# Kernel tuning notes

Measured on AMD Instinct MI355X. Metric: run time of the kernel, lower is better.

Reference implementation:

```python
import jax, jax.numpy as jnp
import numpy as np


def setup_inputs() -> dict:
    key = jax.random.key(0)
    k1, k2 = jax.random.split(key)
    B, N, M = 8, 8192, 8192
    source_points = jax.random.normal(k1, (B, N, 3), dtype=jnp.float32)
    target_points = jax.random.normal(k2, (B, M, 3), dtype=jnp.float32)
    return {"source_points": source_points, "target_points": target_points}


def reference(source_points, target_points):
    # dist: [B, N, M]  (same math as (x[:, :, None] - y[:, None]) ** 2 summed over coords)
    s_sq = jnp.sum(source_points ** 2, axis=-1)  # [B, N]
    t_sq = jnp.sum(target_points ** 2, axis=-1)  # [B, M]
    cross = jnp.einsum("bnd,bmd->bnm", source_points, target_points)  # [B, N, M]
    dist = s_sq[:, :, None] + t_sq[:, None, :] - 2.0 * cross
    min_s2t = jnp.min(dist, axis=2)  # [B, N] nearest target for each source point
    min_t2s = jnp.min(dist, axis=1)  # [B, M] nearest source for each target point
    chamfer = jnp.mean(min_s2t, axis=1) + jnp.mean(min_t2s, axis=1)  # [B]
    return chamfer
```

## Files before the change

kernel.cpp:

```cpp
#include <hip/hip_runtime.h>


typedef float f32x16 __attribute__((ext_vector_type(16)));
typedef short bf16x8 __attribute__((ext_vector_type(8)));

constexpr int BATCH  = 8;
constexpr int NPTS   = 8192;
constexpr int BLOCK  = 256;
constexpr int QTILE  = 256;
constexpr int NAF    = 2;
constexpr int QB     = NPTS / QTILE;
constexpr int DSPLIT = 4;
constexpr int DBR    = NPTS / DSPLIT;
constexpr int NT     = DBR / 32;
constexpr int NBLK   = QB * BATCH * 2 * DSPLIT;

constexpr size_t FRAG_N = (size_t)BATCH * NPTS * 2;
constexpr size_t SM_N   = (size_t)BATCH * NPTS;

static __device__ __forceinline__ unsigned umin2(unsigned a, unsigned b) {
    return a < b ? a : b;
}
static __device__ __forceinline__ unsigned umin3(unsigned a, unsigned b, unsigned c) {
    return umin2(a, umin2(b, c));
}
static __device__ __forceinline__ unsigned short bf16h(float f) {
    unsigned int u = __float_as_uint(f);
    u += 0x7fffu + ((u >> 16) & 1u);
    return (unsigned short)(u >> 16);
}
static __device__ __forceinline__ float bf16tof(unsigned short h) {
    return __uint_as_float(((unsigned int)h) << 16);
}
static __device__ __forceinline__ unsigned int pack2(unsigned short a, unsigned short b) {
    return (unsigned int)a | ((unsigned int)b << 16);
}

static __device__ __forceinline__ void make_bfrag(float px, float py, float pz,
                                                  uint4& p0, uint4& p1) {
    const unsigned short one = bf16h(1.0f);
    float nx = -px, ny = -py, nz = -pz;
    float ht = 0.5f * fmaf(px, px, fmaf(py, py, pz * pz));
    unsigned short nxh = bf16h(nx), nxl = bf16h(nx - bf16tof(nxh));
    unsigned short nyh = bf16h(ny), nyl = bf16h(ny - bf16tof(nyh));
    unsigned short nzh = bf16h(nz), nzl = bf16h(nz - bf16tof(nzh));
    unsigned short hh = bf16h(ht),  hl = bf16h(ht - bf16tof(hh));
    p0 = make_uint4(pack2(nxh, nxl), pack2(nxh, nyh),
                    pack2(nyl, nyh), pack2(nzh, nzl));
    p1 = make_uint4(pack2(nzh, one), pack2(one, hh),
                    pack2(hl, one), 0u);
}

__global__ __launch_bounds__(BLOCK) void chamfer_prep(
    const float* __restrict__ src, const float* __restrict__ tgt,
    uint4* __restrict__ fragS, uint4* __restrict__ fragT,
    unsigned int* __restrict__ mins, float* __restrict__ out)
{
    const int i = blockIdx.x * BLOCK + threadIdx.x;
    uint4 p0, p1;
    const float* tp = tgt + (size_t)i * 3;
    make_bfrag(tp[0], tp[1], tp[2], p0, p1);
    fragT[2 * i + 0] = p0;
    fragT[2 * i + 1] = p1;
    const float* sp = src + (size_t)i * 3;
    make_bfrag(sp[0], sp[1], sp[2], p0, p1);
    fragS[2 * i + 0] = p0;
    fragS[2 * i + 1] = p1;
    mins[i]        = 0x7f7f7f7fu;
    mins[SM_N + i] = 0x7f7f7f7fu;
    if (i < BATCH) out[i] = 0.0f;
}

__global__ __launch_bounds__(BLOCK, 2) void chamfer_nn(
    const float* __restrict__ src, const float* __restrict__ tgt,
    const uint4* __restrict__ fragS, const uint4* __restrict__ fragT,
    unsigned int* __restrict__ mins)
{
    const int tid  = threadIdx.x;
    const int lane = tid & 63;
    const int w    = tid >> 6;
    const int half = lane >> 5;
    const int l31  = lane & 31;

    const int lin  = blockIdx.x;
    const int rest = lin >> 3;
    const int qb   = rest & 31;
    const int p    = ((rest >> 5) << 3) | (lin & 7);
    const int b    = p & 7;
    const int z    = p >> 3;
    const int dir  = z >> 2;
    const int ds   = z & 3;

    const float* P  = dir ? tgt : src;
    const uint4* FB = dir ? fragS : fragT;

    const unsigned short one = bf16h(1.0f);
    bf16x8 af[NAF];
#pragma unroll
    for (int g = 0; g < NAF; g++) {
        const int q = qb * QTILE + w * (32 * NAF) + g * 32 + l31;
        const float* qp = P + ((size_t)b * NPTS + q) * 3;
        float qx = qp[0], qy = qp[1], qz = qp[2];
        float hq = 0.5f * fmaf(qx, qx, fmaf(qy, qy, qz * qz));
        unsigned short xh = bf16h(qx), xl = bf16h(qx - bf16tof(xh));
        unsigned short yh = bf16h(qy), yl = bf16h(qy - bf16tof(yh));
        unsigned short zh = bf16h(qz), zl = bf16h(qz - bf16tof(zh));
        unsigned short qh = bf16h(hq), ql = bf16h(hq - bf16tof(qh));
        bf16x8 a;
        if (half == 0) {
            a[0] = (short)xh; a[1] = (short)xh; a[2] = (short)xl;
            a[3] = (short)yh; a[4] = (short)yh; a[5] = (short)yl;
            a[6] = (short)zh; a[7] = (short)zh;
        } else {
            a[0] = (short)zl; a[1] = (short)qh; a[2] = (short)ql;
            a[3] = (short)one; a[4] = (short)one;
            a[5] = (short)one;
            a[6] = 0; a[7] = 0;
        }
        af[g] = a;
    }

    unsigned rmn0[16], rmn1[16];
#pragma unroll
    for (int r = 0; r < 16; r++) { rmn0[r] = 0x7f7f7f7fu; rmn1[r] = 0x7f7f7f7fu; }
    const f32x16 zz = {};

    const uint4* gp = FB + ((size_t)b * NPTS + (size_t)ds * DBR) * 2
                         + 2 * l31 + half;

    uint4 c0 = gp[0], c1 = gp[64];
    for (int t = 0; t < NT; t += 2) {
        bf16x8 b0 = __builtin_bit_cast(bf16x8, c0);
        bf16x8 b1 = __builtin_bit_cast(bf16x8, c1);
        if (t + 2 < NT) {
            c0 = gp[64 * (t + 2)];
            c1 = gp[64 * (t + 3)];
        }
        f32x16 a00 = __builtin_amdgcn_mfma_f32_32x32x16_bf16(af[0], b0, zz, 0, 0, 0);
        f32x16 a01 = __builtin_amdgcn_mfma_f32_32x32x16_bf16(af[0], b1, zz, 0, 0, 0);
        f32x16 a10 = __builtin_amdgcn_mfma_f32_32x32x16_bf16(af[1], b0, zz, 0, 0, 0);
        f32x16 a11 = __builtin_amdgcn_mfma_f32_32x32x16_bf16(af[1], b1, zz, 0, 0, 0);
#pragma unroll
        for (int r = 0; r < 16; r++) {
            rmn0[r] = umin3(rmn0[r], __float_as_uint(a00[r]), __float_as_uint(a01[r]));
            rmn1[r] = umin3(rmn1[r], __float_as_uint(a10[r]), __float_as_uint(a11[r]));
        }
    }

    unsigned int* M = mins + ((size_t)dir * BATCH + b) * NPTS;
    const int qbase = qb * QTILE + w * (32 * NAF);
#pragma unroll
    for (int r = 0; r < 16; r++) {
        unsigned a = rmn0[r], bv = rmn1[r];
#pragma unroll
        for (int off = 16; off > 0; off >>= 1) {
            a  = umin2(a,  (unsigned)__shfl_xor((int)a,  off, 64));
            bv = umin2(bv, (unsigned)__shfl_xor((int)bv, off, 64));
        }
        if (l31 == 0) {
            const int row = (r & 3) + 8 * (r >> 2) + 4 * half;
            atomicMin(&M[qbase + row],      a);
            atomicMin(&M[qbase + 32 + row], bv);
        }
    }
}

__global__ __launch_bounds__(BLOCK) void chamfer_final(
    const unsigned int* __restrict__ mins, float* __restrict__ out)
{
    const int seg = blockIdx.x;
    const int b   = blockIdx.y;
    const int tid = threadIdx.x;
    float acc = 0.0f;
#pragma unroll
    for (int k = 0; k < 8; k++) {
        const size_t i = (size_t)b * NPTS + seg * 2048 + k * BLOCK + tid;
        acc += fmaxf(__uint_as_float(mins[i]) - 1.0f, 0.0f)
             + fmaxf(__uint_as_float(mins[SM_N + i]) - 1.0f, 0.0f);
    }
    for (int off = 32; off > 0; off >>= 1) acc += __shfl_down(acc, off, 64);
    __shared__ float wsum[4];
    if ((tid & 63) == 0) wsum[tid >> 6] = acc;
    __syncthreads();
    if (tid == 0)
        atomicAdd(&out[b],
                  (wsum[0] + wsum[1] + wsum[2] + wsum[3]) * (2.0f / (float)NPTS));
}

extern "C" void kernel_launch(void* const* d_in, const int* in_sizes, int n_in,
                              void* d_out, int out_size, void* d_ws, size_t ws_size,
                              hipStream_t stream) {
    const float* src = (const float*)d_in[0];
    const float* tgt = (const float*)d_in[1];
    float* out = (float*)d_out;

    uint4* fragT        = (uint4*)d_ws;
    uint4* fragS        = fragT + FRAG_N;
    unsigned int* mins  = (unsigned int*)(fragS + FRAG_N);

    chamfer_prep<<<BATCH * NPTS / BLOCK, BLOCK, 0, stream>>>(
        src, tgt, fragS, fragT, mins, out);
    chamfer_nn<<<NBLK, BLOCK, 0, stream>>>(
        src, tgt, fragS, fragT, mins);
    chamfer_final<<<dim3(4, BATCH), BLOCK, 0, stream>>>(mins, out);
}
```

Before: 100.2 us.

## Compute both chamfer directions from a single distance pass with column minima

The kernel previously ran two separate passes over the distance matrix, one per direction. It now runs only source-to-target tiles, and also reduces each MFMA tile over its rows to get per-target-column minima. Those minima are merged into a shared-memory array through LDS atomics and then flushed to global memory with atomicMin. This halves the MFMA work and block count, at the cost of extra per-tile min trees, cross-half shuffles, LDS atomics and a shared buffer that may reduce occupancy.

```diff
diff --git a/kernel.cpp b/kernel.cpp
--- a/kernel.cpp
+++ b/kernel.cpp
@@ -13,7 +13,7 @@
 constexpr int DSPLIT = 4;
 constexpr int DBR    = NPTS / DSPLIT;
 constexpr int NT     = DBR / 32;
-constexpr int NBLK   = QB * BATCH * 2 * DSPLIT;
+constexpr int NBLK   = QB * BATCH * DSPLIT;
 
 constexpr size_t FRAG_N = (size_t)BATCH * NPTS * 2;
 constexpr size_t SM_N   = (size_t)BATCH * NPTS;
@@ -24,10 +24,20 @@
 static __device__ __forceinline__ unsigned umin3(unsigned a, unsigned b, unsigned c) {
     return umin2(a, umin2(b, c));
 }
+static __device__ __forceinline__ unsigned u(float f) { return __float_as_uint(f); }
+
+static __device__ __forceinline__ unsigned tree16u(const f32x16& a) {
+    unsigned m = umin3(u(a[0]), u(a[1]), u(a[2]));
+    m = umin3(m, u(a[3]),  u(a[4]));  m = umin3(m, u(a[5]),  u(a[6]));
+    m = umin3(m, u(a[7]),  u(a[8]));  m = umin3(m, u(a[9]),  u(a[10]));
+    m = umin3(m, u(a[11]), u(a[12])); m = umin3(m, u(a[13]), u(a[14]));
+    return umin2(m, u(a[15]));
+}
+
 static __device__ __forceinline__ unsigned short bf16h(float f) {
-    unsigned int u = __float_as_uint(f);
-    u += 0x7fffu + ((u >> 16) & 1u);
-    return (unsigned short)(u >> 16);
+    unsigned int v = __float_as_uint(f);
+    v += 0x7fffu + ((v >> 16) & 1u);
+    return (unsigned short)(v >> 16);
 }
 static __device__ __forceinline__ float bf16tof(unsigned short h) {
     return __uint_as_float(((unsigned int)h) << 16);
@@ -36,46 +46,35 @@
     return (unsigned int)a | ((unsigned int)b << 16);
 }
 
-static __device__ __forceinline__ void make_bfrag(float px, float py, float pz,
-                                                  uint4& p0, uint4& p1) {
+__global__ __launch_bounds__(BLOCK) void chamfer_prep(
+    const float* __restrict__ tgt, uint4* __restrict__ fragT,
+    unsigned int* __restrict__ mins, float* __restrict__ out)
+{
+    const int i = blockIdx.x * BLOCK + threadIdx.x;
     const unsigned short one = bf16h(1.0f);
+    const float* tp = tgt + (size_t)i * 3;
+    float px = tp[0], py = tp[1], pz = tp[2];
     float nx = -px, ny = -py, nz = -pz;
     float ht = 0.5f * fmaf(px, px, fmaf(py, py, pz * pz));
     unsigned short nxh = bf16h(nx), nxl = bf16h(nx - bf16tof(nxh));
     unsigned short nyh = bf16h(ny), nyl = bf16h(ny - bf16tof(nyh));
     unsigned short nzh = bf16h(nz), nzl = bf16h(nz - bf16tof(nzh));
     unsigned short hh = bf16h(ht),  hl = bf16h(ht - bf16tof(hh));
-    p0 = make_uint4(pack2(nxh, nxl), pack2(nxh, nyh),
-                    pack2(nyl, nyh), pack2(nzh, nzl));
-    p1 = make_uint4(pack2(nzh, one), pack2(one, hh),
-                    pack2(hl, one), 0u);
-}
-
-__global__ __launch_bounds__(BLOCK) void chamfer_prep(
-    const float* __restrict__ src, const float* __restrict__ tgt,
-    uint4* __restrict__ fragS, uint4* __restrict__ fragT,
-    unsigned int* __restrict__ mins, float* __restrict__ out)
-{
-    const int i = blockIdx.x * BLOCK + threadIdx.x;
-    uint4 p0, p1;
-    const float* tp = tgt + (size_t)i * 3;
-    make_bfrag(tp[0], tp[1], tp[2], p0, p1);
-    fragT[2 * i + 0] = p0;
-    fragT[2 * i + 1] = p1;
-    const float* sp = src + (size_t)i * 3;
-    make_bfrag(sp[0], sp[1], sp[2], p0, p1);
-    fragS[2 * i + 0] = p0;
-    fragS[2 * i + 1] = p1;
+    fragT[2 * i + 0] = make_uint4(pack2(nxh, nxl), pack2(nxh, nyh),
+                                  pack2(nyl, nyh), pack2(nzh, nzl));
+    fragT[2 * i + 1] = make_uint4(pack2(nzh, one), pack2(one, hh),
+                                  pack2(hl, one), 0u);
     mins[i]        = 0x7f7f7f7fu;
     mins[SM_N + i] = 0x7f7f7f7fu;
     if (i < BATCH) out[i] = 0.0f;
 }
 
 __global__ __launch_bounds__(BLOCK, 2) void chamfer_nn(
-    const float* __restrict__ src, const float* __restrict__ tgt,
-    const uint4* __restrict__ fragS, const uint4* __restrict__ fragT,
+    const float* __restrict__ src, const uint4* __restrict__ fragT,
     unsigned int* __restrict__ mins)
 {
+    __shared__ unsigned sht[DBR];
+
     const int tid  = threadIdx.x;
     const int lane = tid & 63;
     const int w    = tid >> 6;
@@ -87,19 +86,16 @@
     const int qb   = rest & 31;
     const int p    = ((rest >> 5) << 3) | (lin & 7);
     const int b    = p & 7;
-    const int z    = p >> 3;
-    const int dir  = z >> 2;
-    const int ds   = z & 3;
-
-    const float* P  = dir ? tgt : src;
-    const uint4* FB = dir ? fragS : fragT;
+    const int ds   = p >> 3;
+
+    for (int j = tid; j < DBR; j += BLOCK) sht[j] = 0x7f7f7f7fu;
 
     const unsigned short one = bf16h(1.0f);
     bf16x8 af[NAF];
 #pragma unroll
     for (int g = 0; g < NAF; g++) {
         const int q = qb * QTILE + w * (32 * NAF) + g * 32 + l31;
-        const float* qp = P + ((size_t)b * NPTS + q) * 3;
+        const float* qp = src + ((size_t)b * NPTS + q) * 3;
         float qx = qp[0], qy = qp[1], qz = qp[2];
         float hq = 0.5f * fmaf(qx, qx, fmaf(qy, qy, qz * qz));
         unsigned short xh = bf16h(qx), xl = bf16h(qx - bf16tof(xh));
@@ -125,8 +121,10 @@
     for (int r = 0; r < 16; r++) { rmn0[r] = 0x7f7f7f7fu; rmn1[r] = 0x7f7f7f7fu; }
     const f32x16 zz = {};
 
-    const uint4* gp = FB + ((size_t)b * NPTS + (size_t)ds * DBR) * 2
-                         + 2 * l31 + half;
+    const uint4* gp = fragT + ((size_t)b * NPTS + (size_t)ds * DBR) * 2
+                            + 2 * l31 + half;
+
+    __syncthreads();
 
     uint4 c0 = gp[0], c1 = gp[64];
     for (int t = 0; t < NT; t += 2) {
@@ -142,12 +140,20 @@
         f32x16 a11 = __builtin_amdgcn_mfma_f32_32x32x16_bf16(af[1], b1, zz, 0, 0, 0);
 #pragma unroll
         for (int r = 0; r < 16; r++) {
-            rmn0[r] = umin3(rmn0[r], __float_as_uint(a00[r]), __float_as_uint(a01[r]));
-            rmn1[r] = umin3(rmn1[r], __float_as_uint(a10[r]), __float_as_uint(a11[r]));
-        }
-    }
-
-    unsigned int* M = mins + ((size_t)dir * BATCH + b) * NPTS;
+            rmn0[r] = umin3(rmn0[r], u(a00[r]), u(a01[r]));
+            rmn1[r] = umin3(rmn1[r], u(a10[r]), u(a11[r]));
+        }
+        unsigned t0 = umin2(tree16u(a00), tree16u(a10));
+        unsigned t1 = umin2(tree16u(a01), tree16u(a11));
+        t0 = umin2(t0, (unsigned)__shfl_xor((int)t0, 32, 64));
+        t1 = umin2(t1, (unsigned)__shfl_xor((int)t1, 32, 64));
+        if (half == 0) {
+            atomicMin(&sht[t * 32 + l31],       t0);
+            atomicMin(&sht[(t + 1) * 32 + l31], t1);
+        }
+    }
+
+    unsigned int* M0 = mins + (size_t)b * NPTS;
     const int qbase = qb * QTILE + w * (32 * NAF);
 #pragma unroll
     for (int r = 0; r < 16; r++) {
@@ -159,10 +165,15 @@
         }
         if (l31 == 0) {
             const int row = (r & 3) + 8 * (r >> 2) + 4 * half;
-            atomicMin(&M[qbase + row],      a);
-            atomicMin(&M[qbase + 32 + row], bv);
-        }
-    }
+            atomicMin(&M0[qbase + row],      a);
+            atomicMin(&M0[qbase + 32 + row], bv);
+        }
+    }
+
+    __syncthreads();
+    unsigned int* M1 = mins + SM_N + (size_t)b * NPTS + (size_t)ds * DBR;
+    for (int j = tid; j < DBR; j += BLOCK)
+        atomicMin(&M1[j], sht[j]);
 }
 
 __global__ __launch_bounds__(BLOCK) void chamfer_final(
@@ -195,12 +206,10 @@
     float* out = (float*)d_out;
 
     uint4* fragT        = (uint4*)d_ws;
-    uint4* fragS        = fragT + FRAG_N;
-    unsigned int* mins  = (unsigned int*)(fragS + FRAG_N);
+    unsigned int* mins  = (unsigned int*)(fragT + FRAG_N);
 
     chamfer_prep<<<BATCH * NPTS / BLOCK, BLOCK, 0, stream>>>(
-        src, tgt, fragS, fragT, mins, out);
-    chamfer_nn<<<NBLK, BLOCK, 0, stream>>>(
-        src, tgt, fragS, fragT, mins);
+        tgt, fragT, mins, out);
+    chamfer_nn<<<NBLK, BLOCK, 0, stream>>>(src, fragT, mins);
     chamfer_final<<<dim3(4, BATCH), BLOCK, 0, stream>>>(mins, out);
 }
```

Result: faster. 96.95 us (-3.2%).
